# Kernel optimization log

Measured on AMD Instinct MI355X. Metric: run time of the kernel, lower is better.

The kernel has to match this reference:

```python
import jax, jax.numpy as jnp
import numpy as np

N_IMG, C_IN, H, W = 8, 8, 136, 200
N_INST = 512
CHANNELS = 8
STRIDE = 8
MASK_OUT_STRIDE = 4
# sizes_of_interest + [last*2], per __init__
SOI = jnp.asarray([64.0, 128.0, 256.0, 512.0, 1024.0, 2048.0], dtype=jnp.float32)
W_NUMS = [(C_IN + 2) * CHANNELS, CHANNELS * CHANNELS, CHANNELS]
B_NUMS = [CHANNELS, CHANNELS, 1]
N_PARAMS = sum(W_NUMS) + sum(B_NUMS)  # 169


def compute_locations(h, w, stride):
    # matches adet compute_locations: centers of stride-sized cells, (x, y)
    shifts_x = jnp.arange(w, dtype=jnp.float32) * stride + stride // 2
    shifts_y = jnp.arange(h, dtype=jnp.float32) * stride + stride // 2
    ys, xs = jnp.meshgrid(shifts_y, shifts_x, indexing='ij')
    return jnp.stack([xs.reshape(-1), ys.reshape(-1)], axis=1)  # [h*w, 2]


def bilinear_up_align_corners(x, out_h, out_w):
    # x: [n, h, w]; F.interpolate(mode='bilinear', align_corners=True)
    n, h, w = x.shape
    ys = jnp.linspace(0.0, h - 1.0, out_h)
    xs = jnp.linspace(0.0, w - 1.0, out_w)
    y0 = jnp.floor(ys).astype(jnp.int32)
    x0 = jnp.floor(xs).astype(jnp.int32)
    y1 = jnp.minimum(y0 + 1, h - 1)
    x1 = jnp.minimum(x0 + 1, w - 1)
    wy = (ys - y0.astype(jnp.float32))[None, :, None]
    wx = (xs - x0.astype(jnp.float32))[None, None, :]
    top = x[:, y0, :]
    bot = x[:, y1, :]
    row0 = top[:, :, x0] * (1.0 - wx) + top[:, :, x1] * wx
    row1 = bot[:, :, x0] * (1.0 - wx) + bot[:, :, x1] * wx
    return row0 * (1.0 - wy) + row1 * wy


def dice_coefficient(x, target):
    eps = 1e-5
    n = x.shape[0]
    x = x.reshape(n, -1)
    target = target.reshape(n, -1)
    intersection = jnp.sum(x * target, axis=1)
    union = jnp.sum(x * x, axis=1) + jnp.sum(target * target, axis=1) + eps
    return 1.0 - 2.0 * intersection / union


def setup_inputs() -> dict:
    key = jax.random.key(0)
    ks = jax.random.split(key, 6)
    mask_feats = jax.random.normal(ks[0], (N_IMG, C_IN, H, W), jnp.float32)
    mask_head_params = jax.random.normal(ks[1], (N_INST, N_PARAMS), jnp.float32) * 0.1
    instance_locations = jax.random.uniform(ks[2], (N_INST, 2), jnp.float32) * jnp.asarray(
        [W * STRIDE, H * STRIDE], dtype=jnp.float32)
    gt_masks = (jax.random.uniform(ks[3], (N_INST, 2 * H, 2 * W), jnp.float32) > 0.5).astype(jnp.float32)
    im_inds = jax.random.randint(ks[4], (N_INST,), 0, N_IMG, jnp.int32)
    fpn_levels = jax.random.randint(ks[5], (N_INST,), 0, 5, jnp.int32)
    return {
        'mask_feats': mask_feats,
        'mask_head_params': mask_head_params,
        'instance_locations': instance_locations,
        'gt_masks': gt_masks,
        'im_inds': im_inds,
        'fpn_levels': fpn_levels,
        'mask_feat_stride': 8,
    }


def reference(mask_feats, mask_head_params, instance_locations, gt_masks, im_inds, fpn_levels, mask_feat_stride):
    n_inst = mask_head_params.shape[0]
    # relative coordinates: instance center minus every grid location, / size-of-interest
    locations = compute_locations(H, W, mask_feat_stride)          # [H*W, 2]
    rel = instance_locations[:, None, :] - locations[None, :, :]   # [n, H*W, 2]
    rel = jnp.transpose(rel, (0, 2, 1)) / SOI[fpn_levels][:, None, None]
    rel = rel.reshape(n_inst, 2, H, W)
    feats = mask_feats[im_inds]                                    # gather [n, C_IN, H, W]
    x = jnp.concatenate([rel, feats], axis=1)                      # [n, C_IN+2, H, W]

    # parse_dynamic_params: split per-instance params into 1x1 conv weights/biases
    splits = np.cumsum(W_NUMS + B_NUMS)[:-1].tolist()
    p = jnp.split(mask_head_params, splits, axis=1)
    w0 = p[0].reshape(n_inst, CHANNELS, C_IN + 2)
    w1 = p[1].reshape(n_inst, CHANNELS, CHANNELS)
    w2 = p[2].reshape(n_inst, 1, CHANNELS)
    b0, b1, b2 = p[3], p[4], p[5]

    # grouped 1x1 convs (groups = n_inst) == per-instance channel GEMM
    x = jax.nn.relu(jnp.einsum('nchw,noc->nohw', x, w0) + b0[:, :, None, None])
    x = jax.nn.relu(jnp.einsum('nchw,noc->nohw', x, w1) + b1[:, :, None, None])
    logits = jnp.einsum('nchw,noc->nohw', x, w2) + b2[:, :, None, None]  # [n, 1, H, W]

    up = mask_feat_stride // MASK_OUT_STRIDE
    logits_up = bilinear_up_align_corners(logits[:, 0], H * up, W * up)
    scores = jax.nn.sigmoid(logits_up)
    loss = dice_coefficient(scores, gt_masks)                      # [n]
    return loss
```

## Files before the change

### kernel.cpp

```cpp
#include <hip/hip_runtime.h>
#include <math.h>

#define NIMG 8
#define CIN 8
#define Hh 136
#define Ww 200
#define HW (Hh * Ww)
#define OH 272
#define OW 400
#define NINST 512
#define NPAR 169
#define TROWS 34
#define NTILES 8
#define LROWS 19
#define SR 5
#define HPAD 9
#define PART_BYTES ((size_t)NINST * NTILES * 3 * 4)

#define PIN(x) asm volatile("" : "+v"(x))
#define MEMFENCE asm volatile("" ::: "memory")

__device__ __forceinline__ void mlp_tile_2p(
    float* __restrict__ slog, float* __restrict__ hbuf,
    const float* __restrict__ fb0, const float* __restrict__ pp,
    int ly0, int lycnt, int tid,
    const float (&A0)[8], const float (&Ax)[8], const float (&Ay)[8])
{
    for (int r0 = 0; r0 < lycnt; r0 += SR) {
        const int rows = (lycnt - r0 < SR) ? (lycnt - r0) : SR;
        const int npx  = rows * Ww;

        MEMFENCE;
        float Wf[64];
#pragma unroll
        for (int o = 0; o < 8; o++)
#pragma unroll
            for (int c = 0; c < 8; c++) Wf[o * 8 + c] = pp[o * 10 + 2 + c];
#pragma unroll
        for (int i = 0; i < 64; i++) PIN(Wf[i]);

        for (int i = tid; i < npx; i += 256) {
            const int r  = i / Ww;
            const int x  = i - r * Ww;
            const int ya = ly0 + r0 + r;
            const float yf = (float)ya;
            const float xf = (float)x;
            const float* fb = fb0 + ya * Ww + x;
            float f[8];
#pragma unroll
            for (int c = 0; c < 8; c++) f[c] = fb[c * HW];
#pragma unroll
            for (int o = 0; o < 8; o++) {
                const float pre = A0[o] + Ay[o] * yf;
                float a = pre + Ax[o] * xf;
#pragma unroll
                for (int c = 0; c < 8; c++) a += Wf[o * 8 + c] * f[c];
                hbuf[i * HPAD + o] = fmaxf(a, 0.0f);
            }
        }
        __syncthreads();

        MEMFENCE;
        float w1[64], w2[8], b1[8], b2;
#pragma unroll
        for (int k = 0; k < 64; k++) w1[k] = pp[80 + k];
#pragma unroll
        for (int k = 0; k < 8; k++) { w2[k] = pp[144 + k]; b1[k] = pp[160 + k]; }
        b2 = pp[168];
#pragma unroll
        for (int k = 0; k < 64; k++) PIN(w1[k]);
#pragma unroll
        for (int k = 0; k < 8; k++) { PIN(w2[k]); PIN(b1[k]); }
        PIN(b2);

        for (int i = tid; i < npx; i += 256) {
            float h[8];
#pragma unroll
            for (int c = 0; c < 8; c++) h[c] = hbuf[i * HPAD + c];
            float g[8];
#pragma unroll
            for (int o = 0; o < 8; o++) {
                float a = b1[o];
#pragma unroll
                for (int c = 0; c < 8; c++) a += w1[o * 8 + c] * h[c];
                g[o] = fmaxf(a, 0.0f);
            }
            float lg = b2;
#pragma unroll
            for (int c = 0; c < 8; c++) lg += w2[c] * g[c];
            slog[r0 * Ww + i] = lg;
        }
        __syncthreads();
    }
}

__device__ __forceinline__ void dice_tile(
    const float* __restrict__ slog, const float* __restrict__ gtn,
    int oy0, int ly0, int lycnt, int tid,
    float& aI, float& aS, float& aT)
{
    const float sy = 135.0f / 271.0f;
    const float sx = 199.0f / 399.0f;
    for (int g4 = tid; g4 < TROWS * (OW / 4); g4 += 256) {
        const int ry = g4 / 100;
        const int gx = (g4 - ry * 100) * 4;
        const int oy = oy0 + ry;
        const float ysf = (float)oy * sy;
        const int y0 = (int)ysf;
        const float wy = ysf - (float)y0;
        const int y1 = (y0 + 1 > Hh - 1) ? (Hh - 1) : (y0 + 1);
        int r0i = y0 - ly0, r1i = y1 - ly0;
        r0i = r0i < 0 ? 0 : (r0i > lycnt - 1 ? lycnt - 1 : r0i);
        r1i = r1i < 0 ? 0 : (r1i > lycnt - 1 ? lycnt - 1 : r1i);
        const float* s0 = &slog[r0i * Ww];
        const float* s1 = &slog[r1i * Ww];

        const float4 t4 = *reinterpret_cast<const float4*>(gtn + ry * OW + gx);
        const float tv[4] = { t4.x, t4.y, t4.z, t4.w };
#pragma unroll
        for (int p = 0; p < 4; p++) {
            const int ox = gx + p;
            const float xsf = (float)ox * sx;
            const int x0 = (int)xsf;
            const float wx = xsf - (float)x0;
            const int x1 = (x0 + 1 > Ww - 1) ? (Ww - 1) : (x0 + 1);
            const float v00 = s0[x0];
            const float v01 = s0[x1];
            const float v10 = s1[x0];
            const float v11 = s1[x1];
            const float top = v00 + wx * (v01 - v00);
            const float bot = v10 + wx * (v11 - v10);
            const float v   = top + wy * (bot - top);
            const float s   = __fdividef(1.0f, 1.0f + __expf(-v));
            aI += s * tv[p];
            aS += s * s;
            aT += tv[p];
        }
    }
}

#define LOAD_AFFINE                                                             \
    const float ix = iloc[2 * n + 0];                                           \
    const float iy = iloc[2 * n + 1];                                           \
    const int   im = iminds[n];                                                 \
    const float invsoi = 1.0f / (float)(64 << lvls[n]);                         \
    const float* pp = pars + n * NPAR;                                          \
    float A0[8], Ax[8], Ay[8];                                                  \
    _Pragma("unroll")                                                           \
    for (int o = 0; o < 8; o++) {                                               \
        const float wx0 = pp[o * 10 + 0];                                       \
        const float wy0 = pp[o * 10 + 1];                                       \
        Ax[o] = -8.0f * invsoi * wx0;                                           \
        Ay[o] = -8.0f * invsoi * wy0;                                           \
        A0[o] = pp[152 + o] + (wx0 * (ix - 4.0f) + wy0 * (iy - 4.0f)) * invsoi; \
    }                                                                           \
    _Pragma("unroll")                                                           \
    for (int o = 0; o < 8; o++) { PIN(A0[o]); PIN(Ax[o]); PIN(Ay[o]); }

__global__ __launch_bounds__(256, 2) void dmh_tile(
    const float* __restrict__ feats,
    const float* __restrict__ pars,
    const float* __restrict__ iloc,
    const float* __restrict__ gt,
    const int* __restrict__ iminds,
    const int* __restrict__ lvls,
    float* __restrict__ part)
{
    __shared__ float slog[LROWS * Ww];
    __shared__ float hbuf[SR * Ww * HPAD];
    __shared__ float sred[12];

    const int n    = blockIdx.y;
    const int tile = blockIdx.x;
    const int tid  = threadIdx.x;

    LOAD_AFFINE

    const float sy = 135.0f / 271.0f;
    const int oy0 = tile * TROWS;
    const int ly0 = (int)((float)oy0 * sy);
    int lyL = (int)((float)(oy0 + TROWS - 1) * sy) + 1;
    if (lyL > Hh - 1) lyL = Hh - 1;
    const int lycnt = lyL - ly0 + 1;

    const float* fb0 = feats + (size_t)im * (CIN * HW);
    mlp_tile_2p(slog, hbuf, fb0, pp, ly0, lycnt, tid, A0, Ax, Ay);

    float aI = 0.0f, aS = 0.0f, aT = 0.0f;
    const float* gtn = gt + (size_t)n * (OH * OW) + (size_t)oy0 * OW;
    dice_tile(slog, gtn, oy0, ly0, lycnt, tid, aI, aS, aT);

#pragma unroll
    for (int off = 32; off > 0; off >>= 1) {
        aI += __shfl_down(aI, off, 64);
        aS += __shfl_down(aS, off, 64);
        aT += __shfl_down(aT, off, 64);
    }
    const int wv = tid >> 6;
    if ((tid & 63) == 0) {
        sred[wv * 3 + 0] = aI;
        sred[wv * 3 + 1] = aS;
        sred[wv * 3 + 2] = aT;
    }
    __syncthreads();
    if (tid == 0) {
        float* pt = part + (size_t)(n * NTILES + tile) * 3;
        pt[0] = sred[0] + sred[3] + sred[6] + sred[9];
        pt[1] = sred[1] + sred[4] + sred[7] + sred[10];
        pt[2] = sred[2] + sred[5] + sred[8] + sred[11];
    }
}

__global__ __launch_bounds__(256) void dmh_fin2(const float* __restrict__ part,
                                                float* __restrict__ out)
{
    const int i = blockIdx.x * 256 + threadIdx.x;
    if (i < NINST) {
        float I = 0.0f, S = 0.0f, T = 0.0f;
#pragma unroll
        for (int t = 0; t < NTILES; t++) {
            const float* pt = part + (size_t)(i * NTILES + t) * 3;
            I += pt[0]; S += pt[1]; T += pt[2];
        }
        out[i] = 1.0f - 2.0f * I / (S + T + 1e-5f);
    }
}

__global__ __launch_bounds__(256, 2) void dmh_one(
    const float* __restrict__ feats,
    const float* __restrict__ pars,
    const float* __restrict__ iloc,
    const float* __restrict__ gt,
    const int* __restrict__ iminds,
    const int* __restrict__ lvls,
    float* __restrict__ out)
{
    __shared__ float slog[LROWS * Ww];
    __shared__ float hbuf[SR * Ww * HPAD];
    __shared__ float sred[12];

    const int n   = blockIdx.x;
    const int tid = threadIdx.x;

    LOAD_AFFINE

    const float sy = 135.0f / 271.0f;
    const float* fb0 = feats + (size_t)im * (CIN * HW);

    float aI = 0.0f, aS = 0.0f, aT = 0.0f;
    for (int tile = 0; tile < NTILES; tile++) {
        const int oy0 = tile * TROWS;
        const int ly0 = (int)((float)oy0 * sy);
        int lyL = (int)((float)(oy0 + TROWS - 1) * sy) + 1;
        if (lyL > Hh - 1) lyL = Hh - 1;
        const int lycnt = lyL - ly0 + 1;

        mlp_tile_2p(slog, hbuf, fb0, pp, ly0, lycnt, tid, A0, Ax, Ay);
        const float* gtn = gt + (size_t)n * (OH * OW) + (size_t)oy0 * OW;
        dice_tile(slog, gtn, oy0, ly0, lycnt, tid, aI, aS, aT);
        __syncthreads();
    }

#pragma unroll
    for (int off = 32; off > 0; off >>= 1) {
        aI += __shfl_down(aI, off, 64);
        aS += __shfl_down(aS, off, 64);
        aT += __shfl_down(aT, off, 64);
    }
    const int wv = tid >> 6;
    if ((tid & 63) == 0) {
        sred[wv * 3 + 0] = aI;
        sred[wv * 3 + 1] = aS;
        sred[wv * 3 + 2] = aT;
    }
    __syncthreads();
    if (tid == 0) {
        const float I = sred[0] + sred[3] + sred[6] + sred[9];
        const float S = sred[1] + sred[4] + sred[7] + sred[10];
        const float T = sred[2] + sred[5] + sred[8] + sred[11];
        out[n] = 1.0f - 2.0f * I / (S + T + 1e-5f);
    }
}

extern "C" void kernel_launch(void* const* d_in, const int* in_sizes, int n_in,
                              void* d_out, int out_size, void* d_ws, size_t ws_size,
                              hipStream_t stream) {
    const float* feats  = (const float*)d_in[0];
    const float* pars   = (const float*)d_in[1];
    const float* iloc   = (const float*)d_in[2];
    const float* gt     = (const float*)d_in[3];
    const int*   iminds = (const int*)d_in[4];
    const int*   lvls   = (const int*)d_in[5];

    if (ws_size >= PART_BYTES) {
        float* part = (float*)d_ws;
        dim3 g(NTILES, NINST);
        dmh_tile<<<g, 256, 0, stream>>>(feats, pars, iloc, gt, iminds, lvls, part);
        dmh_fin2<<<(NINST + 255) / 256, 256, 0, stream>>>(part, (float*)d_out);
    } else {
        dmh_one<<<NINST, 256, 0, stream>>>(feats, pars, iloc, gt, iminds, lvls,
                                           (float*)d_out);
    }
}
```

Before: 478.4 us.

## Vectorize MLP stage to four pixels per thread with planar float4 LDS buffer

Each thread now handles a quad of four adjacent pixels, loading features with float4 global loads and writing hidden activations into a channel-planar shared buffer via float4 stores and loads. Weights are pinned to scalar registers so vector registers stay free, and launch bounds are raised to three blocks per CU. The aim is fewer memory instructions, less per-pixel index arithmetic, and higher occupancy. The risk is more register pressure per thread from the 4-pixel arrays, possible spilling under the tighter bound, and idle threads in the last partial quad chunk.

Result: faster. 400.8 us (-16.2%).

```diff
diff --git a/kernel.cpp b/kernel.cpp
--- a/kernel.cpp
+++ b/kernel.cpp
@@ -13,22 +13,25 @@
 #define TROWS 34
 #define NTILES 8
 #define LROWS 19
-#define SR 5
-#define HPAD 9
+#define SQUADS 256
 #define PART_BYTES ((size_t)NINST * NTILES * 3 * 4)
 
-#define PIN(x) asm volatile("" : "+v"(x))
+#define PINV(x) asm volatile("" : "+v"(x))
+#define PINS(x) asm volatile("" : "+s"(x))
 #define MEMFENCE asm volatile("" ::: "memory")
 
-__device__ __forceinline__ void mlp_tile_2p(
+__device__ __forceinline__ void mlp_tile_2pq(
     float* __restrict__ slog, float* __restrict__ hbuf,
     const float* __restrict__ fb0, const float* __restrict__ pp,
     int ly0, int lycnt, int tid,
     const float (&A0)[8], const float (&Ax)[8], const float (&Ay)[8])
 {
-    for (int r0 = 0; r0 < lycnt; r0 += SR) {
-        const int rows = (lycnt - r0 < SR) ? (lycnt - r0) : SR;
-        const int npx  = rows * Ww;
+    const int tq = lycnt * (Ww / 4);
+    const float* fbase = fb0 + ly0 * Ww;
+
+    for (int q0 = 0; q0 < tq; q0 += SQUADS) {
+        const int q   = q0 + tid;
+        const bool act = q < tq;
 
         MEMFENCE;
         float Wf[64];
@@ -37,58 +40,78 @@
 #pragma unroll
             for (int c = 0; c < 8; c++) Wf[o * 8 + c] = pp[o * 10 + 2 + c];
 #pragma unroll
-        for (int i = 0; i < 64; i++) PIN(Wf[i]);
-
-        for (int i = tid; i < npx; i += 256) {
-            const int r  = i / Ww;
-            const int x  = i - r * Ww;
-            const int ya = ly0 + r0 + r;
-            const float yf = (float)ya;
-            const float xf = (float)x;
-            const float* fb = fb0 + ya * Ww + x;
-            float f[8];
-#pragma unroll
-            for (int c = 0; c < 8; c++) f[c] = fb[c * HW];
+        for (int i = 0; i < 64; i++) PINS(Wf[i]);
+
+        if (act) {
+            const int px = q * 4;
+            const int yy = px / 200;
+            const int x  = px - yy * 200;
+            const float yf = (float)(ly0 + yy);
+            const float* fb = fbase + px;
+            float f[8][4];
+#pragma unroll
+            for (int c = 0; c < 8; c++) {
+                const float4 t = *reinterpret_cast<const float4*>(fb + c * HW);
+                f[c][0] = t.x; f[c][1] = t.y; f[c][2] = t.z; f[c][3] = t.w;
+            }
 #pragma unroll
             for (int o = 0; o < 8; o++) {
                 const float pre = A0[o] + Ay[o] * yf;
-                float a = pre + Ax[o] * xf;
-#pragma unroll
-                for (int c = 0; c < 8; c++) a += Wf[o * 8 + c] * f[c];
-                hbuf[i * HPAD + o] = fmaxf(a, 0.0f);
+                float hv[4];
+#pragma unroll
+                for (int p = 0; p < 4; p++) {
+                    const float xf = (float)(x + p);
+                    float a = pre + Ax[o] * xf;
+#pragma unroll
+                    for (int c = 0; c < 8; c++) a += Wf[o * 8 + c] * f[c][p];
+                    hv[p] = fmaxf(a, 0.0f);
+                }
+                *reinterpret_cast<float4*>(&hbuf[o * (SQUADS * 4) + tid * 4]) =
+                    make_float4(hv[0], hv[1], hv[2], hv[3]);
             }
         }
         __syncthreads();
 
         MEMFENCE;
-        float w1[64], w2[8], b1[8], b2;
+        float w1[64];
 #pragma unroll
         for (int k = 0; k < 64; k++) w1[k] = pp[80 + k];
+#pragma unroll
+        for (int k = 0; k < 64; k++) PINS(w1[k]);
+        float w2[8], b1[8], b2;
 #pragma unroll
         for (int k = 0; k < 8; k++) { w2[k] = pp[144 + k]; b1[k] = pp[160 + k]; }
         b2 = pp[168];
 #pragma unroll
-        for (int k = 0; k < 64; k++) PIN(w1[k]);
-#pragma unroll
-        for (int k = 0; k < 8; k++) { PIN(w2[k]); PIN(b1[k]); }
-        PIN(b2);
-
-        for (int i = tid; i < npx; i += 256) {
-            float h[8];
-#pragma unroll
-            for (int c = 0; c < 8; c++) h[c] = hbuf[i * HPAD + c];
-            float g[8];
-#pragma unroll
-            for (int o = 0; o < 8; o++) {
-                float a = b1[o];
-#pragma unroll
-                for (int c = 0; c < 8; c++) a += w1[o * 8 + c] * h[c];
-                g[o] = fmaxf(a, 0.0f);
+        for (int k = 0; k < 8; k++) { PINV(w2[k]); PINV(b1[k]); }
+        PINV(b2);
+
+        if (act) {
+            float h[8][4];
+#pragma unroll
+            for (int c = 0; c < 8; c++) {
+                const float4 t = *reinterpret_cast<const float4*>(
+                    &hbuf[c * (SQUADS * 4) + tid * 4]);
+                h[c][0] = t.x; h[c][1] = t.y; h[c][2] = t.z; h[c][3] = t.w;
             }
-            float lg = b2;
-#pragma unroll
-            for (int c = 0; c < 8; c++) lg += w2[c] * g[c];
-            slog[r0 * Ww + i] = lg;
+            float o4[4];
+#pragma unroll
+            for (int p = 0; p < 4; p++) {
+                float g[8];
+#pragma unroll
+                for (int o = 0; o < 8; o++) {
+                    float a = b1[o];
+#pragma unroll
+                    for (int c = 0; c < 8; c++) a += w1[o * 8 + c] * h[c][p];
+                    g[o] = fmaxf(a, 0.0f);
+                }
+                float lg = b2;
+#pragma unroll
+                for (int c = 0; c < 8; c++) lg += w2[c] * g[c];
+                o4[p] = lg;
+            }
+            *reinterpret_cast<float4*>(&slog[q * 4]) =
+                make_float4(o4[0], o4[1], o4[2], o4[3]);
         }
         __syncthreads();
     }
@@ -155,9 +178,9 @@
         A0[o] = pp[152 + o] + (wx0 * (ix - 4.0f) + wy0 * (iy - 4.0f)) * invsoi; \
     }                                                                           \
     _Pragma("unroll")                                                           \
-    for (int o = 0; o < 8; o++) { PIN(A0[o]); PIN(Ax[o]); PIN(Ay[o]); }
-
-__global__ __launch_bounds__(256, 2) void dmh_tile(
+    for (int o = 0; o < 8; o++) { PINV(A0[o]); PINV(Ax[o]); PINV(Ay[o]); }
+
+__global__ __launch_bounds__(256, 3) void dmh_tile(
     const float* __restrict__ feats,
     const float* __restrict__ pars,
     const float* __restrict__ iloc,
@@ -167,7 +190,7 @@
     float* __restrict__ part)
 {
     __shared__ float slog[LROWS * Ww];
-    __shared__ float hbuf[SR * Ww * HPAD];
+    __shared__ float hbuf[8 * SQUADS * 4];
     __shared__ float sred[12];
 
     const int n    = blockIdx.y;
@@ -184,7 +207,7 @@
     const int lycnt = lyL - ly0 + 1;
 
     const float* fb0 = feats + (size_t)im * (CIN * HW);
-    mlp_tile_2p(slog, hbuf, fb0, pp, ly0, lycnt, tid, A0, Ax, Ay);
+    mlp_tile_2pq(slog, hbuf, fb0, pp, ly0, lycnt, tid, A0, Ax, Ay);
 
     float aI = 0.0f, aS = 0.0f, aT = 0.0f;
     const float* gtn = gt + (size_t)n * (OH * OW) + (size_t)oy0 * OW;
@@ -226,7 +249,7 @@
     }
 }
 
-__global__ __launch_bounds__(256, 2) void dmh_one(
+__global__ __launch_bounds__(256, 3) void dmh_one(
     const float* __restrict__ feats,
     const float* __restrict__ pars,
     const float* __restrict__ iloc,
@@ -236,7 +259,7 @@
     float* __restrict__ out)
 {
     __shared__ float slog[LROWS * Ww];
-    __shared__ float hbuf[SR * Ww * HPAD];
+    __shared__ float hbuf[8 * SQUADS * 4];
     __shared__ float sred[12];
 
     const int n   = blockIdx.x;
@@ -255,7 +278,7 @@
         if (lyL > Hh - 1) lyL = Hh - 1;
         const int lycnt = lyL - ly0 + 1;
 
-        mlp_tile_2p(slog, hbuf, fb0, pp, ly0, lycnt, tid, A0, Ax, Ay);
+        mlp_tile_2pq(slog, hbuf, fb0, pp, ly0, lycnt, tid, A0, Ax, Ay);
         const float* gtn = gt + (size_t)n * (OH * OW) + (size_t)oy0 * OW;
         dice_tile(slog, gtn, oy0, ly0, lycnt, tid, aI, aS, aT);
         __syncthreads();
```
